# Performance work log

Measured on AMD Instinct MI355X. Metric: run time of the kernel, lower is better.

The kernel has to match this reference:

```python
import jax, jax.numpy as jnp
import numpy as np


def gcn_conv(x, W, b, src, dst, n_nodes):
    """PyG GCNConv: linear transform, then symmetric-normalized sparse aggregation.
    src/dst already include self-loops. Messages flow src -> dst."""
    xw = x @ W  # [N, out]
    deg = jax.ops.segment_sum(jnp.ones_like(dst, dtype=xw.dtype), dst, num_segments=n_nodes)
    dinv = jnp.where(deg > 0, jax.lax.rsqrt(deg), 0.0)
    norm = dinv[src] * dinv[dst]  # [E]
    msg = xw[src] * norm[:, None]  # gather + scale
    out = jax.ops.segment_sum(msg, dst, num_segments=n_nodes)  # scatter-add
    return out + b


def setup_inputs() -> dict:
    key = jax.random.key(0)
    ks = jax.random.split(key, 5)
    N, E, C_in, C_out = 50000, 800000, 512, 128
    H = 2 * C_out
    x = jax.random.normal(ks[0], (N, C_in), dtype=jnp.float32)
    edge_index = jax.random.randint(ks[1], (2, E), 0, N, dtype=jnp.int64)
    def glorot(k, shape):
        lim = float(np.sqrt(6.0 / (shape[0] + shape[1])))
        return jax.random.uniform(k, shape, jnp.float32, -lim, lim)
    return {
        "x": x,
        "edge_index": edge_index,
        "W1": glorot(ks[2], (C_in, H)),
        "b1": jnp.zeros((H,), jnp.float32),
        "W_mu": glorot(ks[3], (H, C_out)),
        "b_mu": jnp.zeros((C_out,), jnp.float32),
        "W_ls": glorot(ks[4], (H, C_out)),
        "b_ls": jnp.zeros((C_out,), jnp.float32),
    }


def reference(x, edge_index, W1, b1, W_mu, b_mu, W_ls, b_ls):
    n_nodes = x.shape[0]
    # add self-loops (PyG GCNConv default add_self_loops=True)
    loops = jnp.arange(n_nodes, dtype=edge_index.dtype)
    src = jnp.concatenate([edge_index[0], loops])
    dst = jnp.concatenate([edge_index[1], loops])
    h = jax.nn.relu(gcn_conv(x, W1, b1, src, dst, n_nodes))
    mu = gcn_conv(h, W_mu, b_mu, src, dst, n_nodes)
    logstd = gcn_conv(h, W_ls, b_ls, src, dst, n_nodes)
    # stack so output is a single array [2, N, out_channels]
    return jnp.stack([mu, logstd])
```

## Files before the change

kernel.cpp:

```cpp
#include <hip/hip_runtime.h>

static inline int ceil_div(int a, int b) { return (a + b - 1) / b; }

typedef __attribute__((ext_vector_type(8))) __bf16 bf16x8;
typedef __attribute__((ext_vector_type(8))) unsigned short ushort8;
typedef __attribute__((ext_vector_type(4))) float f32x4;

__device__ __forceinline__ unsigned short f2bf(float f) {
    union { float f; unsigned u; } v; v.f = f;
    unsigned r = v.u + 0x7fffu + ((v.u >> 16) & 1u);
    return (unsigned short)(r >> 16);
}
__device__ __forceinline__ float blo(unsigned u) {
    union { unsigned u; float f; } x; x.u = u << 16; return x.f;
}
__device__ __forceinline__ float bhi(unsigned u) {
    union { unsigned u; float f; } x; x.u = u & 0xffff0000u; return x.f;
}


__global__ void k_init_cnt(int* __restrict__ cnt, int N) {
    int i = blockIdx.x * blockDim.x + threadIdx.x;
    if (i < N) cnt[i] = 1;
}

__global__ void k_count(const int* __restrict__ dst, int E, int* __restrict__ cnt) {
    int e = blockIdx.x * blockDim.x + threadIdx.x;
    if (e < E) atomicAdd(&cnt[dst[e]], 1);
}

__global__ __launch_bounds__(256) void k_bsum(const int* __restrict__ cnt, int* __restrict__ bsum, int N) {
    __shared__ int ws[4];
    const int i = blockIdx.x * 256 + threadIdx.x;
    const int lane = threadIdx.x & 63, wave = threadIdx.x >> 6;
    int v = (i < N) ? cnt[i] : 0;
    for (int off = 32; off > 0; off >>= 1) v += __shfl_down(v, off);
    if (lane == 0) ws[wave] = v;
    __syncthreads();
    if (threadIdx.x == 0) bsum[blockIdx.x] = ws[0] + ws[1] + ws[2] + ws[3];
}

__global__ __launch_bounds__(256) void k_scan_bsum(const int* __restrict__ bsum, int* __restrict__ bbase,
                                                   int nb, int* __restrict__ row_ptr, int N) {
    __shared__ int ws[4];
    const int tid = threadIdx.x;
    const int lane = tid & 63, wave = tid >> 6;
    const int v = (tid < nb) ? bsum[tid] : 0;
    int x = v;
    for (int off = 1; off < 64; off <<= 1) {
        int t = __shfl_up(x, off);
        if (lane >= off) x += t;
    }
    if (lane == 63) ws[wave] = x;
    __syncthreads();
    if (tid == 0) {
        int r = 0;
        for (int i = 0; i < 4; ++i) { int t = ws[i]; ws[i] = r; r += t; }
        row_ptr[N] = r;
    }
    __syncthreads();
    if (tid < nb) bbase[tid] = ws[wave] + x - v;
}

__global__ __launch_bounds__(256) void k_scan_apply(const int* __restrict__ cnt, const int* __restrict__ bbase,
                                                    int* __restrict__ row_ptr, int* __restrict__ cursor,
                                                    float* __restrict__ dinv, int N) {
    __shared__ int ws[4];
    const int i = blockIdx.x * 256 + threadIdx.x;
    const int lane = threadIdx.x & 63, wave = threadIdx.x >> 6;
    const int c = (i < N) ? cnt[i] : 0;
    int x = c;
    for (int off = 1; off < 64; off <<= 1) {
        int t = __shfl_up(x, off);
        if (lane >= off) x += t;
    }
    if (lane == 63) ws[wave] = x;
    __syncthreads();
    if (threadIdx.x == 0) {
        int r = 0;
        for (int k = 0; k < 4; ++k) { int t = ws[k]; ws[k] = r; r += t; }
    }
    __syncthreads();
    if (i < N) {
        const int excl = bbase[blockIdx.x] + ws[wave] + x - c;
        row_ptr[i] = excl;
        cursor[i] = excl;
        dinv[i] = rsqrtf((float)c);
    }
}

__global__ void k_scatter(const int* __restrict__ src, const int* __restrict__ dst, int E, int N,
                          int* __restrict__ cursor, int* __restrict__ col) {
    int t = blockIdx.x * blockDim.x + threadIdx.x;
    if (t < E) {
        int p = atomicAdd(&cursor[dst[t]], 1);
        col[p] = src[t];
    } else if (t < E + N) {
        int n = t - E;
        int p = atomicAdd(&cursor[n], 1);
        col[p] = n;
    }
}

__global__ void k_prep_w(const float* __restrict__ W1, const float* __restrict__ Wmu,
                         const float* __restrict__ Wls, unsigned short* __restrict__ W1t,
                         unsigned short* __restrict__ Wct, int K1, int H, int Cout) {
    int t = blockIdx.x * blockDim.x + threadIdx.x;
    int n1 = H * K1;
    int n2 = 2 * Cout * H;
    if (t < n1) {
        int c = t / K1, k = t - c * K1;
        W1t[t] = f2bf(W1[(size_t)k * H + c]);
    } else if (t < n1 + n2) {
        int u = t - n1;
        int c = u / H, k = u - c * H;
        float v = (c < Cout) ? Wmu[(size_t)k * Cout + c] : Wls[(size_t)k * Cout + (c - Cout)];
        Wct[u] = f2bf(v);
    }
}

__global__ __launch_bounds__(256) void k_gemm1(const float* __restrict__ x, const unsigned short* __restrict__ W1t,
                                               const float* __restrict__ dinv, unsigned short* __restrict__ y,
                                               int N, int K) {
    __shared__ __align__(16) unsigned short As[64][40];
    const int tid = threadIdx.x;
    const int wave = tid >> 6, lane = tid & 63;
    const int quad = lane >> 4, l16 = lane & 15;
    const int row0 = blockIdx.x * 64;
    const int n0 = wave * 64;
    f32x4 acc[4][4] = {};
    const int sr = tid >> 2;
    const int kc = (tid & 3) * 8;
    const int arow = min(row0 + sr, N - 1);
    const float* ap = x + (size_t)arow * K + kc;
    const unsigned short* bp = W1t + (size_t)(n0 + l16) * K + quad * 8;

    for (int k0 = 0; k0 < K; k0 += 32) {
        float4 a0 = *(const float4*)(ap + k0);
        float4 a1 = *(const float4*)(ap + k0 + 4);
        ushort8 t;
        t[0] = f2bf(a0.x); t[1] = f2bf(a0.y); t[2] = f2bf(a0.z); t[3] = f2bf(a0.w);
        t[4] = f2bf(a1.x); t[5] = f2bf(a1.y); t[6] = f2bf(a1.z); t[7] = f2bf(a1.w);
        *(ushort8*)&As[sr][kc] = t;
        bf16x8 bfr[4];
#pragma unroll
        for (int j = 0; j < 4; ++j) bfr[j] = *(const bf16x8*)(bp + (size_t)j * 16 * K + k0);
        __syncthreads();
#pragma unroll
        for (int i = 0; i < 4; ++i) {
            bf16x8 afr = *(const bf16x8*)&As[i * 16 + l16][quad * 8];
#pragma unroll
            for (int j = 0; j < 4; ++j)
                acc[i][j] = __builtin_amdgcn_mfma_f32_16x16x32_bf16(afr, bfr[j], acc[i][j], 0, 0, 0);
        }
        __syncthreads();
    }
#pragma unroll
    for (int i = 0; i < 4; ++i) {
        const int gr = row0 + i * 16 + quad * 4;
#pragma unroll
        for (int r = 0; r < 4; ++r) {
            const int row = gr + r;
            if (row < N) {
                const float s = dinv[row];
#pragma unroll
                for (int j = 0; j < 4; ++j) {
                    const int gc = n0 + j * 16 + l16;
                    y[(size_t)row * 256 + gc] = f2bf(acc[i][j][r] * s);
                }
            }
        }
    }
}

__global__ __launch_bounds__(256) void k_gemm2(const unsigned short* __restrict__ g,
                                               const unsigned short* __restrict__ Wct,
                                               const float* __restrict__ bmu, const float* __restrict__ bls,
                                               float* __restrict__ out, int N, int Cout) {
    __shared__ __align__(16) unsigned short As[64][40];
    const int K = 256;
    const int tid = threadIdx.x;
    const int wave = tid >> 6, lane = tid & 63;
    const int quad = lane >> 4, l16 = lane & 15;
    const int row0 = blockIdx.x * 64;
    const int n0 = wave * 64;
    f32x4 acc[4][4] = {};
    const int sr = tid >> 2;
    const int kc = (tid & 3) * 8;
    const int arow = min(row0 + sr, N - 1);
    const unsigned short* ap = g + (size_t)arow * K + kc;
    const unsigned short* bp = Wct + (size_t)(n0 + l16) * K + quad * 8;

    for (int k0 = 0; k0 < K; k0 += 32) {
        ushort8 t = *(const ushort8*)(ap + k0);
        *(ushort8*)&As[sr][kc] = t;
        bf16x8 bfr[4];
#pragma unroll
        for (int j = 0; j < 4; ++j) bfr[j] = *(const bf16x8*)(bp + (size_t)j * 16 * K + k0);
        __syncthreads();
#pragma unroll
        for (int i = 0; i < 4; ++i) {
            bf16x8 afr = *(const bf16x8*)&As[i * 16 + l16][quad * 8];
#pragma unroll
            for (int j = 0; j < 4; ++j)
                acc[i][j] = __builtin_amdgcn_mfma_f32_16x16x32_bf16(afr, bfr[j], acc[i][j], 0, 0, 0);
        }
        __syncthreads();
    }
#pragma unroll
    for (int j = 0; j < 4; ++j) {
        const int c = n0 + j * 16 + l16;
        const bool is_mu = (c < Cout);
        const int ocl = is_mu ? c : (c - Cout);
        const float bv = is_mu ? bmu[ocl] : bls[ocl];
        const size_t obase = is_mu ? 0 : (size_t)N * Cout;
#pragma unroll
        for (int i = 0; i < 4; ++i) {
            const int gr = row0 + i * 16 + quad * 4;
#pragma unroll
            for (int r = 0; r < 4; ++r) {
                const int row = gr + r;
                if (row < N) out[obase + (size_t)row * Cout + ocl] = acc[i][j][r] + bv;
            }
        }
    }
}

__global__ __launch_bounds__(256) void k_agg(const unsigned short* __restrict__ Yin,
                                             const int* __restrict__ row_ptr, const int* __restrict__ col,
                                             const float* __restrict__ dinv, const float* __restrict__ bias,
                                             unsigned short* __restrict__ Yout, int N, int relu_mode) {
    const int n = blockIdx.x * 4 + (threadIdx.x >> 6);
    if (n >= N) return;
    const int lane = threadIdx.x & 63;
    const int c = lane * 4;
    const int jb = row_ptr[n], je = row_ptr[n + 1];
    float ax0 = 0.f, ay0 = 0.f, az0 = 0.f, aw0 = 0.f;
    float ax1 = 0.f, ay1 = 0.f, az1 = 0.f, aw1 = 0.f;
    int j = jb;
    for (; j + 3 < je; j += 4) {
        const int s0 = col[j], s1 = col[j + 1], s2 = col[j + 2], s3 = col[j + 3];
        const uint2 v0 = *(const uint2*)(Yin + (size_t)s0 * 256 + c);
        const uint2 v1 = *(const uint2*)(Yin + (size_t)s1 * 256 + c);
        const uint2 v2 = *(const uint2*)(Yin + (size_t)s2 * 256 + c);
        const uint2 v3 = *(const uint2*)(Yin + (size_t)s3 * 256 + c);
        ax0 += blo(v0.x) + blo(v1.x); ay0 += bhi(v0.x) + bhi(v1.x);
        az0 += blo(v0.y) + blo(v1.y); aw0 += bhi(v0.y) + bhi(v1.y);
        ax1 += blo(v2.x) + blo(v3.x); ay1 += bhi(v2.x) + bhi(v3.x);
        az1 += blo(v2.y) + blo(v3.y); aw1 += bhi(v2.y) + bhi(v3.y);
    }
    for (; j < je; ++j) {
        const int s0 = col[j];
        const uint2 v0 = *(const uint2*)(Yin + (size_t)s0 * 256 + c);
        ax0 += blo(v0.x); ay0 += bhi(v0.x); az0 += blo(v0.y); aw0 += bhi(v0.y);
    }
    const float ax = ax0 + ax1, ay = ay0 + ay1, az = az0 + az1, aw = aw0 + aw1;
    const float dn = dinv[n];
    float ox, oy, oz, ow;
    if (relu_mode) {
        const float4 b = *(const float4*)&bias[c];
        ox = fmaxf(dn * ax + b.x, 0.f) * dn;
        oy = fmaxf(dn * ay + b.y, 0.f) * dn;
        oz = fmaxf(dn * az + b.z, 0.f) * dn;
        ow = fmaxf(dn * aw + b.w, 0.f) * dn;
    } else {
        ox = dn * ax; oy = dn * ay; oz = dn * az; ow = dn * aw;
    }
    uint2 o;
    o.x = (unsigned)f2bf(ox) | ((unsigned)f2bf(oy) << 16);
    o.y = (unsigned)f2bf(oz) | ((unsigned)f2bf(ow) << 16);
    *(uint2*)(Yout + (size_t)n * 256 + c) = o;
}


extern "C" void kernel_launch(void* const* d_in, const int* in_sizes, int n_in,
                              void* d_out, int out_size, void* d_ws, size_t ws_size,
                              hipStream_t stream) {
    const float* x   = (const float*)d_in[0];
    const int*   ei  = (const int*)d_in[1];
    const float* W1  = (const float*)d_in[2];
    const float* b1  = (const float*)d_in[3];
    const float* Wmu = (const float*)d_in[4];
    const float* bmu = (const float*)d_in[5];
    const float* Wls = (const float*)d_in[6];
    const float* bls = (const float*)d_in[7];

    const int H    = in_sizes[3];
    const int Cin  = in_sizes[2] / H;
    const int Cout = in_sizes[5];
    const int N    = in_sizes[0] / Cin;
    const int E    = in_sizes[1] / 2;
    const int* srcv = ei;
    const int* dstv = ei + E;

    char* w = (char*)d_ws;
    size_t off = 0;
    auto alloc = [&](size_t bytes) -> void* {
        void* p = w + off;
        off = (off + bytes + 255) & ~(size_t)255;
        return p;
    };
    const int nb = ceil_div(N, 256);
    int*            cnt     = (int*)alloc((size_t)N * 4);
    int*            cursor  = (int*)alloc((size_t)N * 4);
    int*            row_ptr = (int*)alloc((size_t)(N + 1) * 4);
    float*          dinv    = (float*)alloc((size_t)N * 4);
    int*            bsum    = (int*)alloc((size_t)nb * 4);
    int*            bbase   = (int*)alloc((size_t)nb * 4);
    int*            col     = (int*)alloc((size_t)(E + N) * 4);
    unsigned short* W1t     = (unsigned short*)alloc((size_t)H * Cin * 2);
    unsigned short* Wct     = (unsigned short*)alloc((size_t)2 * Cout * H * 2);
    unsigned short* y       = (unsigned short*)alloc((size_t)N * H * 2);
    unsigned short* y2      = (unsigned short*)alloc((size_t)N * H * 2);
    unsigned short* g       = y;
    (void)ws_size; (void)n_in; (void)out_size;

    k_init_cnt<<<ceil_div(N, 256), 256, 0, stream>>>(cnt, N);
    k_count<<<ceil_div(E, 256), 256, 0, stream>>>(dstv, E, cnt);
    k_bsum<<<nb, 256, 0, stream>>>(cnt, bsum, N);
    k_scan_bsum<<<1, 256, 0, stream>>>(bsum, bbase, nb, row_ptr, N);
    k_scan_apply<<<nb, 256, 0, stream>>>(cnt, bbase, row_ptr, cursor, dinv, N);
    k_scatter<<<ceil_div(E + N, 256), 256, 0, stream>>>(srcv, dstv, E, N, cursor, col);
    k_prep_w<<<ceil_div(H * Cin + 2 * Cout * H, 256), 256, 0, stream>>>(W1, Wmu, Wls, W1t, Wct, Cin, H, Cout);

    k_gemm1<<<ceil_div(N, 64), 256, 0, stream>>>(x, W1t, dinv, y, N, Cin);

    k_agg<<<ceil_div(N, 4), 256, 0, stream>>>(y, row_ptr, col, dinv, b1, y2, N, 1);
    k_agg<<<ceil_div(N, 4), 256, 0, stream>>>(y2, row_ptr, col, dinv, nullptr, g, N, 0);

    k_gemm2<<<ceil_div(N, 64), 256, 0, stream>>>(g, Wct, bmu, bls, (float*)d_out, N, Cout);
}
```

Baseline: 462.3 us.

## Merge prep kernels, precast x to bf16, overlap CSR scatter with GEMM1

Folds degree counting, the x-to-bf16 conversion and weight transposition into one multi-role kernel, and replaces the init-count kernel with a memset, adding the self-loop +1 inside the scans. GEMM1 no longer depends on dinv, so its blocks share a launch with the CSR scatter blocks, letting the scatter atomics overlap the matmul. Both GEMMs drop the LDS staging and barriers and load A fragments directly from global bf16. The source-side dinv scaling moves into the aggregation loop as FMAs. This costs an extra bf16 copy of x (write then re-read) and an extra dinv gather per edge.

```diff
diff --git a/kernel.cpp b/kernel.cpp
--- a/kernel.cpp
+++ b/kernel.cpp
@@ -18,22 +18,48 @@
     union { unsigned u; float f; } x; x.u = u & 0xffff0000u; return x.f;
 }
 
-
-__global__ void k_init_cnt(int* __restrict__ cnt, int N) {
-    int i = blockIdx.x * blockDim.x + threadIdx.x;
-    if (i < N) cnt[i] = 1;
-}
-
-__global__ void k_count(const int* __restrict__ dst, int E, int* __restrict__ cnt) {
-    int e = blockIdx.x * blockDim.x + threadIdx.x;
-    if (e < E) atomicAdd(&cnt[dst[e]], 1);
+__global__ __launch_bounds__(256) void k_prep(const int* __restrict__ dst, int E, int* __restrict__ cnt,
+                                              const float* __restrict__ x, unsigned short* __restrict__ xb,
+                                              long nx,
+                                              const float* __restrict__ W1, const float* __restrict__ Wmu,
+                                              const float* __restrict__ Wls, unsigned short* __restrict__ W1t,
+                                              unsigned short* __restrict__ Wct, int K1, int H, int Cout,
+                                              int nbCount, int nbX) {
+    const int b = blockIdx.x;
+    if (b < nbCount) {
+        int e = b * 256 + threadIdx.x;
+        if (e < E) atomicAdd(&cnt[dst[e]], 1);
+    } else if (b < nbCount + nbX) {
+        long i = (long)(b - nbCount) * 2048 + (long)threadIdx.x * 8;
+        if (i < nx) {
+            float4 a0 = *(const float4*)(x + i);
+            float4 a1 = *(const float4*)(x + i + 4);
+            ushort8 t;
+            t[0] = f2bf(a0.x); t[1] = f2bf(a0.y); t[2] = f2bf(a0.z); t[3] = f2bf(a0.w);
+            t[4] = f2bf(a1.x); t[5] = f2bf(a1.y); t[6] = f2bf(a1.z); t[7] = f2bf(a1.w);
+            *(ushort8*)(xb + i) = t;
+        }
+    } else {
+        int t = (b - nbCount - nbX) * 256 + threadIdx.x;
+        int n1 = H * K1;
+        int n2 = 2 * Cout * H;
+        if (t < n1) {
+            int c = t / K1, k = t - c * K1;
+            W1t[t] = f2bf(W1[(size_t)k * H + c]);
+        } else if (t < n1 + n2) {
+            int u = t - n1;
+            int c = u / H, k = u - c * H;
+            float v = (c < Cout) ? Wmu[(size_t)k * Cout + c] : Wls[(size_t)k * Cout + (c - Cout)];
+            Wct[u] = f2bf(v);
+        }
+    }
 }
 
 __global__ __launch_bounds__(256) void k_bsum(const int* __restrict__ cnt, int* __restrict__ bsum, int N) {
     __shared__ int ws[4];
     const int i = blockIdx.x * 256 + threadIdx.x;
     const int lane = threadIdx.x & 63, wave = threadIdx.x >> 6;
-    int v = (i < N) ? cnt[i] : 0;
+    int v = (i < N) ? cnt[i] + 1 : 0;
     for (int off = 32; off > 0; off >>= 1) v += __shfl_down(v, off);
     if (lane == 0) ws[wave] = v;
     __syncthreads();
@@ -68,7 +94,7 @@
     __shared__ int ws[4];
     const int i = blockIdx.x * 256 + threadIdx.x;
     const int lane = threadIdx.x & 63, wave = threadIdx.x >> 6;
-    const int c = (i < N) ? cnt[i] : 0;
+    const int c = (i < N) ? cnt[i] + 1 : 0;
     int x = c;
     for (int off = 1; off < 64; off <<= 1) {
         int t = __shfl_up(x, off);
@@ -89,71 +115,45 @@
     }
 }
 
-__global__ void k_scatter(const int* __restrict__ src, const int* __restrict__ dst, int E, int N,
-                          int* __restrict__ cursor, int* __restrict__ col) {
-    int t = blockIdx.x * blockDim.x + threadIdx.x;
-    if (t < E) {
-        int p = atomicAdd(&cursor[dst[t]], 1);
-        col[p] = src[t];
-    } else if (t < E + N) {
-        int n = t - E;
-        int p = atomicAdd(&cursor[n], 1);
-        col[p] = n;
-    }
-}
-
-__global__ void k_prep_w(const float* __restrict__ W1, const float* __restrict__ Wmu,
-                         const float* __restrict__ Wls, unsigned short* __restrict__ W1t,
-                         unsigned short* __restrict__ Wct, int K1, int H, int Cout) {
-    int t = blockIdx.x * blockDim.x + threadIdx.x;
-    int n1 = H * K1;
-    int n2 = 2 * Cout * H;
-    if (t < n1) {
-        int c = t / K1, k = t - c * K1;
-        W1t[t] = f2bf(W1[(size_t)k * H + c]);
-    } else if (t < n1 + n2) {
-        int u = t - n1;
-        int c = u / H, k = u - c * H;
-        float v = (c < Cout) ? Wmu[(size_t)k * Cout + c] : Wls[(size_t)k * Cout + (c - Cout)];
-        Wct[u] = f2bf(v);
-    }
-}
-
-__global__ __launch_bounds__(256) void k_gemm1(const float* __restrict__ x, const unsigned short* __restrict__ W1t,
-                                               const float* __restrict__ dinv, unsigned short* __restrict__ y,
-                                               int N, int K) {
-    __shared__ __align__(16) unsigned short As[64][40];
+__global__ __launch_bounds__(256) void k_gemm1_scatter(const unsigned short* __restrict__ xb,
+                                                       const unsigned short* __restrict__ W1t,
+                                                       unsigned short* __restrict__ y, int N, int K, int nbGemm,
+                                                       const int* __restrict__ src, const int* __restrict__ dst,
+                                                       int E, int* __restrict__ cursor, int* __restrict__ col) {
+    if (blockIdx.x >= nbGemm) {
+        int t = (blockIdx.x - nbGemm) * 256 + threadIdx.x;
+        if (t < E) {
+            int p = atomicAdd(&cursor[dst[t]], 1);
+            col[p] = src[t];
+        } else if (t < E + N) {
+            int n = t - E;
+            int p = atomicAdd(&cursor[n], 1);
+            col[p] = n;
+        }
+        return;
+    }
     const int tid = threadIdx.x;
     const int wave = tid >> 6, lane = tid & 63;
     const int quad = lane >> 4, l16 = lane & 15;
     const int row0 = blockIdx.x * 64;
     const int n0 = wave * 64;
     f32x4 acc[4][4] = {};
-    const int sr = tid >> 2;
-    const int kc = (tid & 3) * 8;
-    const int arow = min(row0 + sr, N - 1);
-    const float* ap = x + (size_t)arow * K + kc;
+    const unsigned short* ap[4];
+#pragma unroll
+    for (int i = 0; i < 4; ++i) ap[i] = xb + (size_t)min(row0 + i * 16 + l16, N - 1) * K + quad * 8;
     const unsigned short* bp = W1t + (size_t)(n0 + l16) * K + quad * 8;
-
+#pragma unroll 2
     for (int k0 = 0; k0 < K; k0 += 32) {
-        float4 a0 = *(const float4*)(ap + k0);
-        float4 a1 = *(const float4*)(ap + k0 + 4);
-        ushort8 t;
-        t[0] = f2bf(a0.x); t[1] = f2bf(a0.y); t[2] = f2bf(a0.z); t[3] = f2bf(a0.w);
-        t[4] = f2bf(a1.x); t[5] = f2bf(a1.y); t[6] = f2bf(a1.z); t[7] = f2bf(a1.w);
-        *(ushort8*)&As[sr][kc] = t;
-        bf16x8 bfr[4];
+        bf16x8 afr[4], bfr[4];
+#pragma unroll
+        for (int i = 0; i < 4; ++i) afr[i] = *(const bf16x8*)(ap[i] + k0);
 #pragma unroll
         for (int j = 0; j < 4; ++j) bfr[j] = *(const bf16x8*)(bp + (size_t)j * 16 * K + k0);
-        __syncthreads();
-#pragma unroll
-        for (int i = 0; i < 4; ++i) {
-            bf16x8 afr = *(const bf16x8*)&As[i * 16 + l16][quad * 8];
+#pragma unroll
+        for (int i = 0; i < 4; ++i)
 #pragma unroll
             for (int j = 0; j < 4; ++j)
-                acc[i][j] = __builtin_amdgcn_mfma_f32_16x16x32_bf16(afr, bfr[j], acc[i][j], 0, 0, 0);
-        }
-        __syncthreads();
+                acc[i][j] = __builtin_amdgcn_mfma_f32_16x16x32_bf16(afr[i], bfr[j], acc[i][j], 0, 0, 0);
     }
 #pragma unroll
     for (int i = 0; i < 4; ++i) {
@@ -162,12 +162,9 @@
         for (int r = 0; r < 4; ++r) {
             const int row = gr + r;
             if (row < N) {
-                const float s = dinv[row];
-#pragma unroll
-                for (int j = 0; j < 4; ++j) {
-                    const int gc = n0 + j * 16 + l16;
-                    y[(size_t)row * 256 + gc] = f2bf(acc[i][j][r] * s);
-                }
+#pragma unroll
+                for (int j = 0; j < 4; ++j)
+                    y[(size_t)row * 256 + n0 + j * 16 + l16] = f2bf(acc[i][j][r]);
             }
         }
     }
@@ -177,7 +174,6 @@
                                                const unsigned short* __restrict__ Wct,
                                                const float* __restrict__ bmu, const float* __restrict__ bls,
                                                float* __restrict__ out, int N, int Cout) {
-    __shared__ __align__(16) unsigned short As[64][40];
     const int K = 256;
     const int tid = threadIdx.x;
     const int wave = tid >> 6, lane = tid & 63;
@@ -185,27 +181,22 @@
     const int row0 = blockIdx.x * 64;
     const int n0 = wave * 64;
     f32x4 acc[4][4] = {};
-    const int sr = tid >> 2;
-    const int kc = (tid & 3) * 8;
-    const int arow = min(row0 + sr, N - 1);
-    const unsigned short* ap = g + (size_t)arow * K + kc;
+    const unsigned short* ap[4];
+#pragma unroll
+    for (int i = 0; i < 4; ++i) ap[i] = g + (size_t)min(row0 + i * 16 + l16, N - 1) * K + quad * 8;
     const unsigned short* bp = Wct + (size_t)(n0 + l16) * K + quad * 8;
-
+#pragma unroll 2
     for (int k0 = 0; k0 < K; k0 += 32) {
-        ushort8 t = *(const ushort8*)(ap + k0);
-        *(ushort8*)&As[sr][kc] = t;
-        bf16x8 bfr[4];
+        bf16x8 afr[4], bfr[4];
+#pragma unroll
+        for (int i = 0; i < 4; ++i) afr[i] = *(const bf16x8*)(ap[i] + k0);
 #pragma unroll
         for (int j = 0; j < 4; ++j) bfr[j] = *(const bf16x8*)(bp + (size_t)j * 16 * K + k0);
-        __syncthreads();
-#pragma unroll
-        for (int i = 0; i < 4; ++i) {
-            bf16x8 afr = *(const bf16x8*)&As[i * 16 + l16][quad * 8];
+#pragma unroll
+        for (int i = 0; i < 4; ++i)
 #pragma unroll
             for (int j = 0; j < 4; ++j)
-                acc[i][j] = __builtin_amdgcn_mfma_f32_16x16x32_bf16(afr, bfr[j], acc[i][j], 0, 0, 0);
-        }
-        __syncthreads();
+                acc[i][j] = __builtin_amdgcn_mfma_f32_16x16x32_bf16(afr[i], bfr[j], acc[i][j], 0, 0, 0);
     }
 #pragma unroll
     for (int j = 0; j < 4; ++j) {
@@ -240,29 +231,38 @@
     int j = jb;
     for (; j + 3 < je; j += 4) {
         const int s0 = col[j], s1 = col[j + 1], s2 = col[j + 2], s3 = col[j + 3];
+        const float d0 = dinv[s0], d1 = dinv[s1], d2 = dinv[s2], d3 = dinv[s3];
         const uint2 v0 = *(const uint2*)(Yin + (size_t)s0 * 256 + c);
         const uint2 v1 = *(const uint2*)(Yin + (size_t)s1 * 256 + c);
         const uint2 v2 = *(const uint2*)(Yin + (size_t)s2 * 256 + c);
         const uint2 v3 = *(const uint2*)(Yin + (size_t)s3 * 256 + c);
-        ax0 += blo(v0.x) + blo(v1.x); ay0 += bhi(v0.x) + bhi(v1.x);
-        az0 += blo(v0.y) + blo(v1.y); aw0 += bhi(v0.y) + bhi(v1.y);
-        ax1 += blo(v2.x) + blo(v3.x); ay1 += bhi(v2.x) + bhi(v3.x);
-        az1 += blo(v2.y) + blo(v3.y); aw1 += bhi(v2.y) + bhi(v3.y);
+        ax0 = fmaf(d0, blo(v0.x), fmaf(d1, blo(v1.x), ax0));
+        ay0 = fmaf(d0, bhi(v0.x), fmaf(d1, bhi(v1.x), ay0));
+        az0 = fmaf(d0, blo(v0.y), fmaf(d1, blo(v1.y), az0));
+        aw0 = fmaf(d0, bhi(v0.y), fmaf(d1, bhi(v1.y), aw0));
+        ax1 = fmaf(d2, blo(v2.x), fmaf(d3, blo(v3.x), ax1));
+        ay1 = fmaf(d2, bhi(v2.x), fmaf(d3, bhi(v3.x), ay1));
+        az1 = fmaf(d2, blo(v2.y), fmaf(d3, blo(v3.y), az1));
+        aw1 = fmaf(d2, bhi(v2.y), fmaf(d3, bhi(v3.y), aw1));
     }
     for (; j < je; ++j) {
         const int s0 = col[j];
+        const float d0 = dinv[s0];
         const uint2 v0 = *(const uint2*)(Yin + (size_t)s0 * 256 + c);
-        ax0 += blo(v0.x); ay0 += bhi(v0.x); az0 += blo(v0.y); aw0 += bhi(v0.y);
+        ax0 = fmaf(d0, blo(v0.x), ax0);
+        ay0 = fmaf(d0, bhi(v0.x), ay0);
+        az0 = fmaf(d0, blo(v0.y), az0);
+        aw0 = fmaf(d0, bhi(v0.y), aw0);
     }
     const float ax = ax0 + ax1, ay = ay0 + ay1, az = az0 + az1, aw = aw0 + aw1;
     const float dn = dinv[n];
     float ox, oy, oz, ow;
     if (relu_mode) {
         const float4 b = *(const float4*)&bias[c];
-        ox = fmaxf(dn * ax + b.x, 0.f) * dn;
-        oy = fmaxf(dn * ay + b.y, 0.f) * dn;
-        oz = fmaxf(dn * az + b.z, 0.f) * dn;
-        ow = fmaxf(dn * aw + b.w, 0.f) * dn;
+        ox = fmaxf(fmaf(dn, ax, b.x), 0.f);
+        oy = fmaxf(fmaf(dn, ay, b.y), 0.f);
+        oz = fmaxf(fmaf(dn, az, b.z), 0.f);
+        ow = fmaxf(fmaf(dn, aw, b.w), 0.f);
     } else {
         ox = dn * ax; oy = dn * ay; oz = dn * az; ow = dn * aw;
     }
@@ -310,20 +310,29 @@
     int*            col     = (int*)alloc((size_t)(E + N) * 4);
     unsigned short* W1t     = (unsigned short*)alloc((size_t)H * Cin * 2);
     unsigned short* Wct     = (unsigned short*)alloc((size_t)2 * Cout * H * 2);
+    unsigned short* xb      = (unsigned short*)alloc((size_t)N * Cin * 2);
     unsigned short* y       = (unsigned short*)alloc((size_t)N * H * 2);
     unsigned short* y2      = (unsigned short*)alloc((size_t)N * H * 2);
     unsigned short* g       = y;
     (void)ws_size; (void)n_in; (void)out_size;
 
-    k_init_cnt<<<ceil_div(N, 256), 256, 0, stream>>>(cnt, N);
-    k_count<<<ceil_div(E, 256), 256, 0, stream>>>(dstv, E, cnt);
+    hipMemsetAsync(cnt, 0, (size_t)N * 4, stream);
+
+    const long nx = (long)N * Cin;
+    const int nbCount = ceil_div(E, 256);
+    const int nbX = (int)((nx + 2047) / 2048);
+    const int nbW = ceil_div(H * Cin + 2 * Cout * H, 256);
+    k_prep<<<nbCount + nbX + nbW, 256, 0, stream>>>(dstv, E, cnt, x, xb, nx, W1, Wmu, Wls, W1t, Wct,
+                                                    Cin, H, Cout, nbCount, nbX);
+
     k_bsum<<<nb, 256, 0, stream>>>(cnt, bsum, N);
     k_scan_bsum<<<1, 256, 0, stream>>>(bsum, bbase, nb, row_ptr, N);
     k_scan_apply<<<nb, 256, 0, stream>>>(cnt, bbase, row_ptr, cursor, dinv, N);
-    k_scatter<<<ceil_div(E + N, 256), 256, 0, stream>>>(srcv, dstv, E, N, cursor, col);
-    k_prep_w<<<ceil_div(H * Cin + 2 * Cout * H, 256), 256, 0, stream>>>(W1, Wmu, Wls, W1t, Wct, Cin, H, Cout);
-
-    k_gemm1<<<ceil_div(N, 64), 256, 0, stream>>>(x, W1t, dinv, y, N, Cin);
+
+    const int nbGemm = ceil_div(N, 64);
+    const int nbScat = ceil_div(E + N, 256);
+    k_gemm1_scatter<<<nbGemm + nbScat, 256, 0, stream>>>(xb, W1t, y, N, Cin, nbGemm,
+                                                         srcv, dstv, E, cursor, col);
 
     k_agg<<<ceil_div(N, 4), 256, 0, stream>>>(y, row_ptr, col, dinv, b1, y2, N, 1);
     k_agg<<<ceil_div(N, 4), 256, 0, stream>>>(y2, row_ptr, col, dinv, nullptr, g, N, 0);
```

Measured after the change: 478.3 us. 1.03x slower.
